# Performance work log

Hardware: AMD Instinct MI355X
Metric: run time of the kernel (lower is better)

Reference implementation:

```python
import jax, jax.numpy as jnp
import numpy as np

DIM = 2048
DIM_VISUAL = 1024
DIM_HEAD = 64
HEADS = 16
INNER = DIM_HEAD * HEADS  # 1024
B, T, N_MEDIA, N_VIS = 4, 2048, 8, 64
LN_EPS = 1e-5


def setup_inputs() -> dict:
    key = jax.random.key(0)
    ks = jax.random.split(key, 8)
    y = jax.random.normal(ks[0], (B, T, DIM), dtype=jnp.float32)
    media = jax.random.normal(ks[1], (B, N_MEDIA, N_VIS, DIM_VISUAL), dtype=jnp.float32)
    # one <image> token marker every T//N_MEDIA positions so all text tokens attend
    loc = np.zeros((B, T), dtype=bool)
    step = T // N_MEDIA
    loc[:, ::step] = True
    media_locations = jnp.asarray(loc)
    # params (stored as (in, out) for x @ W)
    ln_w = jnp.ones((DIM,), dtype=jnp.float32)
    ln_b = jnp.zeros((DIM,), dtype=jnp.float32)
    Wq = jax.random.normal(ks[2], (DIM, INNER), dtype=jnp.float32) / np.sqrt(DIM)
    Wkv = jax.random.normal(ks[3], (DIM_VISUAL, 2 * INNER), dtype=jnp.float32) / np.sqrt(DIM_VISUAL)
    Wout = jax.random.normal(ks[4], (INNER, DIM), dtype=jnp.float32) / np.sqrt(INNER)
    return {"y": y, "media": media, "media_locations": media_locations,
            "ln_w": ln_w, "ln_b": ln_b, "Wq": Wq, "Wkv": Wkv, "Wout": Wout}


def reference(y, media, media_locations, ln_w, ln_b, Wq, Wkv, Wout):
    scale = DIM_HEAD ** -0.5
    b, t_med, n_vis, _ = media.shape
    n_tok = y.shape[1]
    # LayerNorm
    mu = jnp.mean(y, axis=-1, keepdims=True)
    var = jnp.var(y, axis=-1, keepdims=True)
    yn = (y - mu) * jax.lax.rsqrt(var + LN_EPS) * ln_w + ln_b
    # projections
    q = (yn @ Wq) * scale                                   # [b, t, inner]
    media_f = media.reshape(b, t_med * n_vis, -1)           # [b, j, dv]
    kv = media_f @ Wkv
    k, v = jnp.split(kv, 2, axis=-1)                        # [b, j, inner]
    def split_heads(x):
        return x.reshape(x.shape[0], x.shape[1], HEADS, DIM_HEAD).transpose(0, 2, 1, 3)
    q, k, v = split_heads(q), split_heads(k), split_heads(v)  # [b, h, n, d]
    sim = jnp.einsum('bhid,bhjd->bhij', q, k)               # [b, h, t, j]
    # media-location block mask
    text_time = jnp.cumsum(media_locations.astype(jnp.int32), axis=-1)  # [b, t]
    media_time = jnp.repeat(jnp.arange(1, t_med + 1), n_vis)            # [j]
    mask = text_time[:, None, :, None] == media_time[None, None, None, :]
    neg = -jnp.finfo(sim.dtype).max
    sim = jnp.where(mask, sim, neg)
    alphas = jax.nn.softmax(sim, axis=-1)
    out = jnp.einsum('bhij,bhjd->bhid', alphas, v)          # [b, h, t, d]
    out = out.transpose(0, 2, 1, 3).reshape(b, n_tok, INNER)
    return out @ Wout
```

## Files before the change

### kernel.cpp

```cpp
#include <hip/hip_runtime.h>

typedef __bf16 bf16x8 __attribute__((ext_vector_type(8)));
typedef float f32x4 __attribute__((ext_vector_type(4)));
typedef int i32x4 __attribute__((ext_vector_type(4)));

#define T_DIM   2048
#define D_MODEL 2048
#define INNER_D 1024
#define N_HEADS 16
#define D_HEAD  64
#define BATCH   4
#define J_TOK   512

__device__ __forceinline__ bool is_bf16(const unsigned short* lnw) {
  return lnw[0] == 0x3F80u;
}

__device__ __forceinline__ void async16(const void* g, void* l) {
  __builtin_amdgcn_global_load_lds(
      (const __attribute__((address_space(1))) void*)g,
      (__attribute__((address_space(3))) void*)l, 16, 0, 0);
}

__device__ __forceinline__ void transpose_tile(const void* in, __bf16* out,
                                               int R, int C, int r0, int c0,
                                               bool isbf, __bf16 (*t)[33]) {
  const int tx = threadIdx.x & 31, ty = threadIdx.x >> 5;
#pragma unroll
  for (int i = 0; i < 4; ++i) {
    const size_t idx = (size_t)(r0 + ty + i * 8) * C + c0 + tx;
    t[ty + i * 8][tx] = isbf ? ((const __bf16*)in)[idx] : (__bf16)((const float*)in)[idx];
  }
  __syncthreads();
#pragma unroll
  for (int i = 0; i < 4; ++i)
    out[(size_t)(c0 + ty + i * 8) * R + r0 + tx] = t[tx][ty + i * 8];
}

__global__ __launch_bounds__(256) void prep_kernel(
    const int* __restrict__ mloc, int* __restrict__ chunk,
    const void* __restrict__ media, __bf16* __restrict__ media_bf,
    const void* __restrict__ Wkv, __bf16* __restrict__ WkvT,
    const void* __restrict__ Wq, __bf16* __restrict__ WqT,
    const unsigned short* __restrict__ lnw) {
  __shared__ int sd[256];
  __shared__ __bf16 t[32][33];
  const bool isbf = is_bf16(lnw);
  const int bid = blockIdx.x;
  const int tid = threadIdx.x;

  if (bid < 4) {
    const int b = bid;
    const int base = tid * 8;
    const int* row = mloc + b * T_DIM;
    int v[8];
    int s = 0;
#pragma unroll
    for (int i = 0; i < 8; ++i) { v[i] = (row[base + i] != 0) ? 1 : 0; s += v[i]; }
    sd[tid] = s;
    __syncthreads();
    for (int off = 1; off < 256; off <<= 1) {
      int tv = (tid >= off) ? sd[tid - off] : 0;
      __syncthreads();
      sd[tid] += tv;
      __syncthreads();
    }
    int run = sd[tid] - s;
#pragma unroll
    for (int i = 0; i < 8; ++i) {
      run += v[i];
      chunk[b * T_DIM + base + i] = run - 1;
    }
  } else if (bid < 4 + 1024) {
    const size_t i = ((size_t)(bid - 4) * 256 + tid) * 8;
    if (isbf) {
      *(i32x4*)(media_bf + i) = *(const i32x4*)((const __bf16*)media + i);
    } else {
      const float* p = (const float*)media + i;
      f32x4 a = *(const f32x4*)p, b2 = *(const f32x4*)(p + 4);
      bf16x8 o;
#pragma unroll
      for (int j = 0; j < 4; ++j) { o[j] = (__bf16)a[j]; o[4 + j] = (__bf16)b2[j]; }
      *(i32x4*)(media_bf + i) = __builtin_bit_cast(i32x4, o);
    }
  } else if (bid < 4 + 1024 + 2048) {
    const int idx = bid - (4 + 1024);
    transpose_tile(Wkv, WkvT, 1024, 2048, (idx >> 6) * 32, (idx & 63) * 32, isbf, t);
  } else {
    const int idx = bid - (4 + 1024 + 2048);
    transpose_tile(Wq, WqT, 2048, 1024, (idx >> 5) * 32, (idx & 31) * 32, isbf, t);
  }
}

__global__ __launch_bounds__(256) void transpose_kernel(const void* __restrict__ in,
                                                        __bf16* __restrict__ out,
                                                        int R, int C,
                                                        const unsigned short* __restrict__ lnw) {
  __shared__ __bf16 t[32][33];
  transpose_tile(in, out, R, C, blockIdx.y * 32, blockIdx.x * 32, is_bf16(lnw), t);
}

__global__ __launch_bounds__(256) void ln_kernel(const void* __restrict__ yv,
                                                 const void* __restrict__ wv_,
                                                 const void* __restrict__ bv_,
                                                 __bf16* __restrict__ yn) {
  const int row = blockIdx.x;
  const int tid = threadIdx.x;
  const int lane = tid & 63, wave = tid >> 6;
  const bool isbf = is_bf16((const unsigned short*)wv_);
  float xf[8], wf[8], bf[8];
  if (isbf) {
    const __bf16* x = (const __bf16*)yv + (size_t)row * D_MODEL + tid * 8;
    bf16x8 xv = __builtin_bit_cast(bf16x8, *(const i32x4*)x);
    bf16x8 ww = __builtin_bit_cast(bf16x8, *(const i32x4*)((const __bf16*)wv_ + tid * 8));
    bf16x8 bb = __builtin_bit_cast(bf16x8, *(const i32x4*)((const __bf16*)bv_ + tid * 8));
#pragma unroll
    for (int i = 0; i < 8; ++i) { xf[i] = (float)xv[i]; wf[i] = (float)ww[i]; bf[i] = (float)bb[i]; }
  } else {
    const float* x = (const float*)yv + (size_t)row * D_MODEL + tid * 8;
    f32x4 a0 = *(const f32x4*)x, a1 = *(const f32x4*)(x + 4);
    const float* wp = (const float*)wv_ + tid * 8;
    f32x4 w0 = *(const f32x4*)wp, w1 = *(const f32x4*)(wp + 4);
    const float* bp = (const float*)bv_ + tid * 8;
    f32x4 b0 = *(const f32x4*)bp, b1 = *(const f32x4*)(bp + 4);
#pragma unroll
    for (int i = 0; i < 4; ++i) {
      xf[i] = a0[i]; xf[4 + i] = a1[i];
      wf[i] = w0[i]; wf[4 + i] = w1[i];
      bf[i] = b0[i]; bf[4 + i] = b1[i];
    }
  }
  float s = 0.f, s2 = 0.f;
#pragma unroll
  for (int i = 0; i < 8; ++i) { s += xf[i]; s2 += xf[i] * xf[i]; }
#pragma unroll
  for (int off = 32; off > 0; off >>= 1) { s += __shfl_xor(s, off); s2 += __shfl_xor(s2, off); }
  __shared__ float red[4][2];
  if (lane == 0) { red[wave][0] = s; red[wave][1] = s2; }
  __syncthreads();
  s = red[0][0] + red[1][0] + red[2][0] + red[3][0];
  s2 = red[0][1] + red[1][1] + red[2][1] + red[3][1];
  const float mu = s * (1.f / D_MODEL);
  const float var = s2 * (1.f / D_MODEL) - mu * mu;
  const float rstd = rsqrtf(var + 1e-5f);
  bf16x8 outv;
#pragma unroll
  for (int i = 0; i < 8; ++i)
    outv[i] = (__bf16)((xf[i] - mu) * rstd * wf[i] + bf[i]);
  *(i32x4*)(yn + (size_t)row * D_MODEL + tid * 8) = __builtin_bit_cast(i32x4, outv);
}

__global__ __launch_bounds__(256) void gemm_bt(const __bf16* __restrict__ A,
                                               const __bf16* __restrict__ Bt,
                                               void* __restrict__ Cv,
                                               int M, int N, int K, float alpha,
                                               int cF, const unsigned short* __restrict__ lnw) {
  __shared__ __bf16 As[128 * 64];
  __shared__ __bf16 Bs[128 * 64];
  const int tid = threadIdx.x;
  const int wave = tid >> 6, lane = tid & 63;
  const int wrow = wave & 1, wcol = wave >> 1;
  const int bm0 = blockIdx.y * 128, bn0 = blockIdx.x * 128;
  const int lr = lane & 15, qd = lane >> 4;

  int r_[4], j_[4];
#pragma unroll
  for (int i = 0; i < 4; ++i) {
    int u = i * 256 + tid;
    r_[i] = u >> 3;
    j_[i] = ((u & 7) - (u >> 3)) & 7;
  }

  f32x4 acc[4][4] = {};

  for (int k0 = 0; k0 < K; k0 += 64) {
#pragma unroll
    for (int i = 0; i < 4; ++i)
      async16(A + (size_t)(bm0 + r_[i]) * K + k0 + j_[i] * 8, &As[(i * 256 + tid) * 8]);
#pragma unroll
    for (int i = 0; i < 4; ++i)
      async16(Bt + (size_t)(bn0 + r_[i]) * K + k0 + j_[i] * 8, &Bs[(i * 256 + tid) * 8]);
    __syncthreads();

#pragma unroll
    for (int ks = 0; ks < 2; ++ks) {
      bf16x8 af[4], bf[4];
#pragma unroll
      for (int mt = 0; mt < 4; ++mt) {
        int row = wrow * 64 + mt * 16 + lr;
        int c = ks * 4 + qd;
        af[mt] = *(const bf16x8*)&As[row * 64 + ((c + row) & 7) * 8];
      }
#pragma unroll
      for (int nt = 0; nt < 4; ++nt) {
        int row = wcol * 64 + nt * 16 + lr;
        int c = ks * 4 + qd;
        bf[nt] = *(const bf16x8*)&Bs[row * 64 + ((c + row) & 7) * 8];
      }
#pragma unroll
      for (int mt = 0; mt < 4; ++mt)
#pragma unroll
        for (int nt = 0; nt < 4; ++nt)
          acc[mt][nt] =
              __builtin_amdgcn_mfma_f32_16x16x32_bf16(af[mt], bf[nt], acc[mt][nt], 0, 0, 0);
    }
    __syncthreads();
  }

  const int r0w = qd * 4, cn = lr;
  const bool f32out = cF && !is_bf16(lnw);
  if (!f32out) {
    __bf16* C = (__bf16*)Cv;
#pragma unroll
    for (int mt = 0; mt < 4; ++mt)
#pragma unroll
      for (int nt = 0; nt < 4; ++nt)
#pragma unroll
        for (int r = 0; r < 4; ++r) {
          int grow = bm0 + wrow * 64 + mt * 16 + r0w + r;
          int gcol = bn0 + wcol * 64 + nt * 16 + cn;
          C[(size_t)grow * N + gcol] = (__bf16)(acc[mt][nt][r] * alpha);
        }
  } else {
    float* C = (float*)Cv;
#pragma unroll
    for (int mt = 0; mt < 4; ++mt)
#pragma unroll
      for (int nt = 0; nt < 4; ++nt)
#pragma unroll
        for (int r = 0; r < 4; ++r) {
          int grow = bm0 + wrow * 64 + mt * 16 + r0w + r;
          int gcol = bn0 + wcol * 64 + nt * 16 + cn;
          C[(size_t)grow * N + gcol] = acc[mt][nt][r] * alpha;
        }
  }
}

__global__ __launch_bounds__(256) void attn_kernel(const __bf16* __restrict__ q,
                                                   const __bf16* __restrict__ kv,
                                                   const int* __restrict__ chunk,
                                                   __bf16* __restrict__ attn) {
  const int h = blockIdx.x, tile = blockIdx.y, b = blockIdx.z;
  const int tid = threadIdx.x, wave = tid >> 6, lane = tid & 63;
  const int lr = lane & 15, qd = lane >> 4;
  __shared__ __bf16 Vt[64][72];
  __shared__ __bf16 P[4][64][72];

  int c = chunk[b * T_DIM + tile * 256];
  c = c < 0 ? 0 : (c > 7 ? 7 : c);
  const size_t kvbase = ((size_t)b * J_TOK + c * 64) * (2 * INNER_D);

#pragma unroll
  for (int it = 0; it < 2; ++it) {
    int u = it * 256 + tid;
    int key = u & 63, d0 = (u >> 6) * 8;
    bf16x8 v = __builtin_bit_cast(
        bf16x8, *(const i32x4*)(kv + kvbase + (size_t)key * (2 * INNER_D) + INNER_D + h * 64 + d0));
#pragma unroll
    for (int j = 0; j < 8; ++j) Vt[d0 + j][key] = v[j];
  }
  __syncthreads();

  const size_t qbase = ((size_t)(b * T_DIM + tile * 256 + wave * 64)) * INNER_D + h * 64;
  f32x4 acc[4][4] = {};
#pragma unroll
  for (int ks = 0; ks < 2; ++ks) {
    bf16x8 af[4], bf[4];
#pragma unroll
    for (int mt = 0; mt < 4; ++mt)
      af[mt] = __builtin_bit_cast(
          bf16x8, *(const i32x4*)(q + qbase + (size_t)(mt * 16 + lr) * INNER_D + ks * 32 + qd * 8));
#pragma unroll
    for (int nt = 0; nt < 4; ++nt)
      bf[nt] = __builtin_bit_cast(
          bf16x8,
          *(const i32x4*)(kv + kvbase + (size_t)(nt * 16 + lr) * (2 * INNER_D) + h * 64 + ks * 32 + qd * 8));
#pragma unroll
    for (int mt = 0; mt < 4; ++mt)
#pragma unroll
      for (int nt = 0; nt < 4; ++nt)
        acc[mt][nt] =
            __builtin_amdgcn_mfma_f32_16x16x32_bf16(af[mt], bf[nt], acc[mt][nt], 0, 0, 0);
  }

#pragma unroll
  for (int mt = 0; mt < 4; ++mt) {
#pragma unroll
    for (int r = 0; r < 4; ++r) {
      float v0 = acc[mt][0][r], v1 = acc[mt][1][r], v2 = acc[mt][2][r], v3 = acc[mt][3][r];
      float mx = fmaxf(fmaxf(v0, v1), fmaxf(v2, v3));
      mx = fmaxf(mx, __shfl_xor(mx, 1));
      mx = fmaxf(mx, __shfl_xor(mx, 2));
      mx = fmaxf(mx, __shfl_xor(mx, 4));
      mx = fmaxf(mx, __shfl_xor(mx, 8));
      float p0 = __expf(v0 - mx), p1 = __expf(v1 - mx), p2 = __expf(v2 - mx), p3 = __expf(v3 - mx);
      float l = p0 + p1 + p2 + p3;
      l += __shfl_xor(l, 1);
      l += __shfl_xor(l, 2);
      l += __shfl_xor(l, 4);
      l += __shfl_xor(l, 8);
      const float rl = 1.0f / l;
      const int row = mt * 16 + qd * 4 + r;
      P[wave][row][lr]      = (__bf16)(p0 * rl);
      P[wave][row][16 + lr] = (__bf16)(p1 * rl);
      P[wave][row][32 + lr] = (__bf16)(p2 * rl);
      P[wave][row][48 + lr] = (__bf16)(p3 * rl);
    }
  }
  __syncthreads();

  f32x4 oc[4][4] = {};
#pragma unroll
  for (int ks = 0; ks < 2; ++ks) {
    bf16x8 af[4], bv[4];
#pragma unroll
    for (int mt = 0; mt < 4; ++mt)
      af[mt] = *(const bf16x8*)&P[wave][mt * 16 + lr][ks * 32 + qd * 8];
#pragma unroll
    for (int nt = 0; nt < 4; ++nt)
      bv[nt] = *(const bf16x8*)&Vt[nt * 16 + lr][ks * 32 + qd * 8];
#pragma unroll
    for (int mt = 0; mt < 4; ++mt)
#pragma unroll
      for (int nt = 0; nt < 4; ++nt)
        oc[mt][nt] =
            __builtin_amdgcn_mfma_f32_16x16x32_bf16(af[mt], bv[nt], oc[mt][nt], 0, 0, 0);
  }

#pragma unroll
  for (int mt = 0; mt < 4; ++mt)
#pragma unroll
    for (int nt = 0; nt < 4; ++nt)
#pragma unroll
      for (int r = 0; r < 4; ++r) {
        int row = mt * 16 + qd * 4 + r;
        int col = nt * 16 + lr;
        attn[((size_t)(b * T_DIM + tile * 256 + wave * 64 + row)) * INNER_D + h * 64 + col] =
            (__bf16)oc[mt][nt][r];
      }
}

extern "C" void kernel_launch(void* const* d_in, const int* in_sizes, int n_in,
                              void* d_out, int out_size, void* d_ws, size_t ws_size,
                              hipStream_t stream) {
  const void* y     = d_in[0];
  const void* media = d_in[1];
  const int*  mloc  = (const int*)d_in[2];
  const unsigned short* lnw = (const unsigned short*)d_in[3];
  const void* lnb   = d_in[4];
  const void* Wq    = d_in[5];
  const void* Wkv   = d_in[6];
  const void* Wout  = d_in[7];

  char* ws = (char*)d_ws;
  int*    chunk    = (int*)ws;
  __bf16* yn       = (__bf16*)(ws + 65536);
  __bf16* media_bf = yn;
  __bf16* WkvT     = (__bf16*)(ws + 65536 + 4194304);
  __bf16* attn     = yn;
  __bf16* q        = (__bf16*)(ws + 65536 + 33554432);
  __bf16* WoutT    = q;
  __bf16* kv       = (__bf16*)(ws + 65536 + 33554432 + 16777216);
  __bf16* WqT      = (__bf16*)(ws + 65536 + 33554432 + 16777216 + 8388608);

  prep_kernel<<<4 + 1024 + 2048 + 2048, 256, 0, stream>>>(
      mloc, chunk, media, media_bf, Wkv, WkvT, Wq, WqT, lnw);
  gemm_bt<<<dim3(16, 16), 256, 0, stream>>>(media_bf, WkvT, kv, 2048, 2048, 1024, 1.0f, 0, lnw);
  ln_kernel<<<BATCH * T_DIM, 256, 0, stream>>>(y, lnw, lnb, yn);
  gemm_bt<<<dim3(8, 64), 256, 0, stream>>>(yn, WqT, q, 8192, 1024, 2048, 0.125f, 0, lnw);
  attn_kernel<<<dim3(16, 8, 4), 256, 0, stream>>>(q, kv, chunk, attn);
  transpose_kernel<<<dim3(64, 32), 256, 0, stream>>>(Wout, WoutT, 1024, 2048, lnw);
  gemm_bt<<<dim3(16, 64), 256, 0, stream>>>(attn, WoutT, d_out, 8192, 2048, 1024, 1.0f, 1, lnw);
}
```

Before: 291.2 us.

## Add 256x256-tile 8-wave pipelined GEMM for the output projection

Adds a new GEMM kernel with 256x256 block tiles, 512 threads, XOR-swizzled LDS, and double-buffered async global-to-LDS loads. Loads are interleaved with MFMA phases using barriers and setprio. It replaces the 128-tile gemm_bt for the final attn @ Wout projection, aiming for more operand reuse and better overlap of loads with MFMA work. The trade-off is 128KB of LDS per block and only 256 blocks, so each CU holds at most one block, which risks poor latency hiding and lower occupancy.

```diff
diff --git a/kernel.cpp b/kernel.cpp
--- a/kernel.cpp
+++ b/kernel.cpp
@@ -232,6 +232,186 @@
           int grow = bm0 + wrow * 64 + mt * 16 + r0w + r;
           int gcol = bn0 + wcol * 64 + nt * 16 + cn;
           C[(size_t)grow * N + gcol] = acc[mt][nt][r] * alpha;
+        }
+  }
+}
+
+__device__ __forceinline__ bf16x8 fragld(const __bf16* half, int row, int cb) {
+  int off = row * 128 + cb;
+  off ^= ((off >> 9) & 1) << 5;
+  return *(const bf16x8*)((const char*)half + off);
+}
+
+__global__ __launch_bounds__(512, 2) void gemm256(const __bf16* __restrict__ A,
+                                                  const __bf16* __restrict__ Bt,
+                                                  void* __restrict__ Cv,
+                                                  int M, int N, int K, float alpha,
+                                                  int cF, const unsigned short* __restrict__ lnw) {
+  __shared__ __bf16 lds[8][128 * 64];
+  const int tid = threadIdx.x;
+  const int wave = tid >> 6, lane = tid & 63;
+  const int wm = wave >> 2, wn = wave & 3;
+  const int lr = lane & 15, qd = lane >> 4;
+  const int bm0 = blockIdx.y * 256, bn0 = blockIdx.x * 256;
+  const int nt = K >> 6;
+
+  int rS[2], cS[2];
+#pragma unroll
+  for (int q = 0; q < 2; ++q) {
+    int p = (q * 512 + tid) * 16;
+    int lp = p ^ (((p >> 9) & 1) << 5);
+    rS[q] = lp >> 7;
+    cS[q] = (lp & 127) >> 1;
+  }
+  const __bf16* sA[2][2];
+  const __bf16* sB[2][2];
+#pragma unroll
+  for (int h = 0; h < 2; ++h)
+#pragma unroll
+    for (int q = 0; q < 2; ++q) {
+      sA[h][q] = A + (size_t)(bm0 + h * 128 + rS[q]) * K + cS[q];
+      sB[h][q] = Bt + (size_t)(bn0 + h * 128 + rS[q]) * K + cS[q];
+    }
+  const int d0 = tid * 16, d1 = (512 + tid) * 16;
+
+#define STG(sp, half, k)                         \
+  do {                                           \
+    async16((sp)[0] + (k), (char*)(half) + d0);  \
+    async16((sp)[1] + (k), (char*)(half) + d1);  \
+  } while (0)
+
+  STG(sB[0], lds[2], 0);
+  STG(sA[0], lds[0], 0);
+  STG(sB[1], lds[3], 0);
+  STG(sA[1], lds[1], 0);
+  if (nt > 1) {
+    STG(sB[0], lds[6], 64);
+    STG(sA[0], lds[4], 64);
+    asm volatile("s_waitcnt vmcnt(4)" ::: "memory");
+  } else {
+    asm volatile("s_waitcnt vmcnt(0)" ::: "memory");
+  }
+  __builtin_amdgcn_sched_barrier(0);
+  __builtin_amdgcn_s_barrier();
+
+  f32x4 acc[8][4] = {};
+  bf16x8 af[4][2], bf[4][2];
+  const int brow = (wn & 1) * 64;
+
+  for (int t = 0; t < nt; ++t) {
+    const int bs = (t & 1) << 2, nb = bs ^ 4;
+    const __bf16* myA = lds[bs + wm];
+    const __bf16* myB = lds[bs + 2 + (wn >> 1)];
+    const int k1 = (t + 1) << 6, k2 = (t + 2) << 6;
+
+#pragma unroll
+    for (int m = 0; m < 4; ++m)
+#pragma unroll
+      for (int ks = 0; ks < 2; ++ks)
+        af[m][ks] = fragld(myA, m * 16 + lr, ks * 64 + qd * 16);
+#pragma unroll
+    for (int n = 0; n < 2; ++n)
+#pragma unroll
+      for (int ks = 0; ks < 2; ++ks)
+        bf[n][ks] = fragld(myB, brow + n * 16 + lr, ks * 64 + qd * 16);
+    if (t + 1 < nt) STG(sB[1], lds[nb + 3], k1);
+    __builtin_amdgcn_s_barrier();
+    __builtin_amdgcn_s_setprio(1);
+#pragma unroll
+    for (int m = 0; m < 4; ++m)
+#pragma unroll
+      for (int n = 0; n < 2; ++n)
+#pragma unroll
+        for (int ks = 0; ks < 2; ++ks)
+          acc[m][n] =
+              __builtin_amdgcn_mfma_f32_16x16x32_bf16(af[m][ks], bf[n][ks], acc[m][n], 0, 0, 0);
+    __builtin_amdgcn_s_setprio(0);
+    __builtin_amdgcn_s_barrier();
+
+#pragma unroll
+    for (int n = 0; n < 2; ++n)
+#pragma unroll
+      for (int ks = 0; ks < 2; ++ks)
+        bf[2 + n][ks] = fragld(myB, brow + (2 + n) * 16 + lr, ks * 64 + qd * 16);
+    if (t + 1 < nt) STG(sA[1], lds[nb + 1], k1);
+    __builtin_amdgcn_s_barrier();
+    __builtin_amdgcn_s_setprio(1);
+#pragma unroll
+    for (int m = 0; m < 4; ++m)
+#pragma unroll
+      for (int n = 0; n < 2; ++n)
+#pragma unroll
+        for (int ks = 0; ks < 2; ++ks)
+          acc[m][2 + n] = __builtin_amdgcn_mfma_f32_16x16x32_bf16(af[m][ks], bf[2 + n][ks],
+                                                                  acc[m][2 + n], 0, 0, 0);
+    __builtin_amdgcn_s_setprio(0);
+    __builtin_amdgcn_s_barrier();
+
+#pragma unroll
+    for (int m = 0; m < 4; ++m)
+#pragma unroll
+      for (int ks = 0; ks < 2; ++ks)
+        af[m][ks] = fragld(myA, 64 + m * 16 + lr, ks * 64 + qd * 16);
+    if (t + 2 < nt) STG(sB[0], lds[bs + 2], k2);
+    __builtin_amdgcn_s_barrier();
+    __builtin_amdgcn_s_setprio(1);
+#pragma unroll
+    for (int m = 0; m < 4; ++m)
+#pragma unroll
+      for (int n = 0; n < 2; ++n)
+#pragma unroll
+        for (int ks = 0; ks < 2; ++ks)
+          acc[4 + m][2 + n] = __builtin_amdgcn_mfma_f32_16x16x32_bf16(
+              af[m][ks], bf[2 + n][ks], acc[4 + m][2 + n], 0, 0, 0);
+    __builtin_amdgcn_s_setprio(0);
+    __builtin_amdgcn_s_barrier();
+
+    if (t + 2 < nt) STG(sA[0], lds[bs + 0], k2);
+    __builtin_amdgcn_s_barrier();
+    __builtin_amdgcn_s_setprio(1);
+#pragma unroll
+    for (int m = 0; m < 4; ++m)
+#pragma unroll
+      for (int n = 0; n < 2; ++n)
+#pragma unroll
+        for (int ks = 0; ks < 2; ++ks)
+          acc[4 + m][n] = __builtin_amdgcn_mfma_f32_16x16x32_bf16(af[m][ks], bf[n][ks],
+                                                                  acc[4 + m][n], 0, 0, 0);
+    __builtin_amdgcn_s_setprio(0);
+    if (t + 2 < nt) {
+      asm volatile("s_waitcnt vmcnt(4)" ::: "memory");
+    } else {
+      asm volatile("s_waitcnt vmcnt(0)" ::: "memory");
+    }
+    __builtin_amdgcn_sched_barrier(0);
+    __builtin_amdgcn_s_barrier();
+  }
+#undef STG
+
+  const bool f32out = cF && !is_bf16(lnw);
+  if (!f32out) {
+    __bf16* C = (__bf16*)Cv;
+#pragma unroll
+    for (int m = 0; m < 8; ++m)
+#pragma unroll
+      for (int n = 0; n < 4; ++n)
+#pragma unroll
+        for (int r = 0; r < 4; ++r) {
+          int grow = bm0 + wm * 128 + m * 16 + qd * 4 + r;
+          int gcol = bn0 + wn * 64 + n * 16 + lr;
+          C[(size_t)grow * N + gcol] = (__bf16)(acc[m][n][r] * alpha);
+        }
+  } else {
+    float* C = (float*)Cv;
+#pragma unroll
+    for (int m = 0; m < 8; ++m)
+#pragma unroll
+      for (int n = 0; n < 4; ++n)
+#pragma unroll
+        for (int r = 0; r < 4; ++r) {
+          int grow = bm0 + wm * 128 + m * 16 + qd * 4 + r;
+          int gcol = bn0 + wn * 64 + n * 16 + lr;
+          C[(size_t)grow * N + gcol] = acc[m][n][r] * alpha;
         }
   }
 }
@@ -370,5 +550,5 @@
   gemm_bt<<<dim3(8, 64), 256, 0, stream>>>(yn, WqT, q, 8192, 1024, 2048, 0.125f, 0, lnw);
   attn_kernel<<<dim3(16, 8, 4), 256, 0, stream>>>(q, kv, chunk, attn);
   transpose_kernel<<<dim3(64, 32), 256, 0, stream>>>(Wout, WoutT, 1024, 2048, lnw);
-  gemm_bt<<<dim3(16, 64), 256, 0, stream>>>(attn, WoutT, d_out, 8192, 2048, 1024, 1.0f, 1, lnw);
-}
+  gemm256<<<dim3(8, 32), 512, 0, stream>>>(attn, WoutT, d_out, 8192, 2048, 1024, 1.0f, 1, lnw);
+}
```

Result: no change. 288.4 us (-1.0%).
